# Performance work log

Measured on AMD Instinct MI355X. Metric: run time of the kernel, lower is better.

The kernel has to match this reference:

```python
import jax, jax.numpy as jnp
import numpy as np

NODE_DIM = 128
N_NODES = 100000
N_EDGES = 600000


def setup_inputs() -> dict:
    key = jax.random.key(0)
    k_x, k_e, k_w1, k_b1, k_w2, k_b2 = jax.random.split(key, 6)
    x = jax.random.normal(k_x, (N_NODES, NODE_DIM), dtype=jnp.float32)
    edge_index = jax.random.randint(k_e, (2, N_EDGES), 0, N_NODES, dtype=jnp.int64)
    # nn.Linear default init: U(-1/sqrt(fan_in), 1/sqrt(fan_in))
    lim1 = 1.0 / np.sqrt(2 * NODE_DIM)
    W1 = jax.random.uniform(k_w1, (2 * NODE_DIM, NODE_DIM), minval=-lim1, maxval=lim1, dtype=jnp.float32)
    b1 = jax.random.uniform(k_b1, (NODE_DIM,), minval=-lim1, maxval=lim1, dtype=jnp.float32)
    lim2 = 1.0 / np.sqrt(NODE_DIM)
    W2 = jax.random.uniform(k_w2, (NODE_DIM, 1), minval=-lim2, maxval=lim2, dtype=jnp.float32)
    b2 = jax.random.uniform(k_b2, (1,), minval=-lim2, maxval=lim2, dtype=jnp.float32)
    return {"x": x, "edge_index": edge_index, "W1": W1, "b1": b1, "W2": W2, "b2": b2}


def reference(x, edge_index, W1, b1, W2, b2):
    src = edge_index[0]
    dst = edge_index[1]
    # [E, 2*node_dim] gathered pair features
    pair = jnp.concatenate([x[src], x[dst]], axis=-1)
    h = jax.nn.relu(pair @ W1 + b1)          # [E, node_dim]
    s = jax.nn.sigmoid(h @ W2 + b2)          # [E, 1]
    return s.squeeze(-1)                      # [E]
```

## Files before the change

kernel.cpp:

```cpp
#include <hip/hip_runtime.h>
#include <hip/hip_bf16.h>
#include <stdint.h>

#define NODE_DIM 128
#define N_NODES  100000
#define N_EDGES  600000
#define NOUT     256

#define QSTEP_INV 64.0f
#define QSTEP     (1.0f / 64.0f)

typedef __bf16 bf16x8 __attribute__((ext_vector_type(8)));
typedef float  f32x4  __attribute__((ext_vector_type(4)));

static __device__ inline unsigned pack2_bf16(float a, float b) {
    unsigned short ua = __builtin_bit_cast(unsigned short, (__bf16)a);
    unsigned short ub = __builtin_bit_cast(unsigned short, (__bf16)b);
    return (unsigned)ua | ((unsigned)ub << 16);
}

static __device__ __forceinline__ void async_copy16(const float* g, void* l) {
    __builtin_amdgcn_global_load_lds(
        (__attribute__((address_space(1))) void*)(uintptr_t)g,
        (__attribute__((address_space(3))) void*)(uint32_t)(uintptr_t)l,
        16, 0, 0);
}

__global__ void wprep_kernel(const float* __restrict__ W1, __bf16* __restrict__ Wt) {
    int i = blockIdx.x * 256 + threadIdx.x;
    if (i >= NOUT * NODE_DIM) return;
    int kp = i >> 7;
    int n  = i & 127;
    float v = W1[i];
    int np = (kp < NODE_DIM) ? n  : (n + NODE_DIM);
    int k  = (kp < NODE_DIM) ? kp : (kp - NODE_DIM);
    Wt[np * NODE_DIM + k] = (__bf16)v;
}

#define MT   64
#define ELD  264

__global__ __launch_bounds__(256)
void gemm_pre_kernel(const float* __restrict__ x, const __bf16* __restrict__ Wt,
                     const float* __restrict__ b1,
                     unsigned char* __restrict__ Ai, unsigned char* __restrict__ Bi) {
    __shared__ __align__(16) char lds_raw[MT * ELD * 2];
    float* Xf = (float*)lds_raw;
    __bf16 (*Ls)[ELD] = (__bf16 (*)[ELD])lds_raw;

    const int t    = threadIdx.x;
    const int wave = t >> 6;
    const int lane = t & 63;
    const int lm   = lane & 15;
    const int q    = lane >> 4;
    const int m0   = blockIdx.x * MT;
    const int n0   = wave * 64;

#pragma unroll
    for (int i = 0; i < 8; ++i) {
        const int sbase = i * 256 + wave * 64;
        const int s  = sbase + lane;
        const int R  = s >> 5;
        const int p  = s & 31;
        const int cg = p ^ (R & 7);
        int gr = m0 + R;
        if (gr > N_NODES - 1) gr = N_NODES - 1;
        async_copy16(x + (size_t)gr * NODE_DIM + cg * 4, &Xf[(size_t)sbase * 4]);
    }

    bf16x8 bfr[4][4];
#pragma unroll
    for (int nt = 0; nt < 4; ++nt) {
        const int n = n0 + nt * 16 + lm;
#pragma unroll
        for (int ks = 0; ks < 4; ++ks)
            bfr[nt][ks] = __builtin_bit_cast(bf16x8,
                *(const uint4*)(Wt + (size_t)n * NODE_DIM + ks * 32 + q * 8));
    }

    __syncthreads();

    f32x4 acc[4][4];
#pragma unroll
    for (int i = 0; i < 4; ++i)
#pragma unroll
        for (int j = 0; j < 4; ++j)
            acc[i][j] = (f32x4){0.f, 0.f, 0.f, 0.f};

#pragma unroll
    for (int mt = 0; mt < 4; ++mt) {
        const int R  = mt * 16 + lm;
        const int rs = R & 7;
#pragma unroll
        for (int ks = 0; ks < 4; ++ks) {
            const int c0 = ks * 8 + q * 2;
            const float4 f0 = *(const float4*)&Xf[(R * 32 + (c0 ^ rs)) * 4];
            const float4 f1 = *(const float4*)&Xf[(R * 32 + ((c0 + 1) ^ rs)) * 4];
            uint4 p;
            p.x = pack2_bf16(f0.x, f0.y);
            p.y = pack2_bf16(f0.z, f0.w);
            p.z = pack2_bf16(f1.x, f1.y);
            p.w = pack2_bf16(f1.z, f1.w);
            bf16x8 af = __builtin_bit_cast(bf16x8, p);
#pragma unroll
            for (int nt = 0; nt < 4; ++nt)
                acc[mt][nt] = __builtin_amdgcn_mfma_f32_16x16x32_bf16(
                    af, bfr[nt][ks], acc[mt][nt], 0, 0, 0);
        }
    }

    __syncthreads();

#pragma unroll
    for (int nt = 0; nt < 4; ++nt) {
        const int n = n0 + nt * 16 + lm;
        const float bias = (n < NODE_DIM) ? b1[n] : 0.f;
#pragma unroll
        for (int mt = 0; mt < 4; ++mt) {
#pragma unroll
            for (int r = 0; r < 4; ++r)
                Ls[mt * 16 + q * 4 + r][n] = (__bf16)(acc[mt][nt][r] + bias);
        }
    }
    __syncthreads();

    const int grp = t >> 4;
    const int sub = t & 15;
#pragma unroll
    for (int pass = 0; pass < 8; ++pass) {
        const int hr   = pass * 16 + grp;
        const int row  = hr >> 1;
        const int half = hr & 1;
        const uint4 v = *(const uint4*)(&Ls[row][half * 128 + sub * 8]);
        const unsigned* vu = (const unsigned*)&v;
        unsigned u[8];
#pragma unroll
        for (int i = 0; i < 4; ++i) {
            const float fa = __builtin_bit_cast(float, vu[i] << 16);
            const float fb = __builtin_bit_cast(float, vu[i] & 0xffff0000u);
            float ga = fmaf(fa, QSTEP_INV, 128.5f);
            float gb = fmaf(fb, QSTEP_INV, 128.5f);
            ga = fminf(fmaxf(ga, 0.f), 255.f);
            gb = fminf(fmaxf(gb, 0.f), 255.f);
            u[2 * i]     = (unsigned)ga;
            u[2 * i + 1] = (unsigned)gb;
        }
        uint2 pk;
        pk.x = u[0] | (u[1] << 8) | (u[2] << 16) | (u[3] << 24);
        pk.y = u[4] | (u[5] << 8) | (u[6] << 16) | (u[7] << 24);
        const int m = m0 + row;
        if (m < N_NODES)
            *(uint2*)((half ? Bi : Ai) + (size_t)m * NODE_DIM + sub * 8) = pk;
    }
}

__global__ __launch_bounds__(256)
void edge_score_kernel(const unsigned char* __restrict__ Ai,
                       const unsigned char* __restrict__ Bi,
                       const int* __restrict__ idx,
                       const float* __restrict__ W2, const float* __restrict__ b2,
                       float* __restrict__ out) {
    const int t      = threadIdx.x;
    const int sub    = t & 15;
    const int g0     = (blockIdx.x * 256 + t) >> 4;
    const int stride = (gridDim.x * 256) >> 4;

    float w[8];
#pragma unroll
    for (int j = 0; j < 8; ++j) w[j] = W2[sub * 8 + j];
    const float bias2 = b2[0];

    for (int e = g0; e < N_EDGES; e += 2 * stride) {
        const int e1  = e + stride;
        const bool h1 = e1 < N_EDGES;
        const int s0 = idx[e];
        const int d0 = idx[N_EDGES + e];
        const int s1 = h1 ? idx[e1] : s0;
        const int d1 = h1 ? idx[N_EDGES + e1] : d0;

        const uint2 a0 = *(const uint2*)(Ai + (size_t)s0 * NODE_DIM + sub * 8);
        const uint2 b0 = *(const uint2*)(Bi + (size_t)d0 * NODE_DIM + sub * 8);
        const uint2 a1 = *(const uint2*)(Ai + (size_t)s1 * NODE_DIM + sub * 8);
        const uint2 b1v= *(const uint2*)(Bi + (size_t)d1 * NODE_DIM + sub * 8);

        const unsigned aw0[2] = {a0.x, a0.y}, bw0[2] = {b0.x, b0.y};
        const unsigned aw1[2] = {a1.x, a1.y}, bw1[2] = {b1v.x, b1v.y};
        float p0 = 0.f, p1 = 0.f;
#pragma unroll
        for (int wd = 0; wd < 2; ++wd) {
#pragma unroll
            for (int k = 0; k < 4; ++k) {
                const int ua0 = (int)((aw0[wd] >> (8 * k)) & 0xffu);
                const int ub0 = (int)((bw0[wd] >> (8 * k)) & 0xffu);
                const int ua1 = (int)((aw1[wd] >> (8 * k)) & 0xffu);
                const int ub1 = (int)((bw1[wd] >> (8 * k)) & 0xffu);
                const int r0 = max(ua0 + ub0, 256) - 256;
                const int r1 = max(ua1 + ub1, 256) - 256;
                p0 = fmaf((float)r0, w[wd * 4 + k], p0);
                p1 = fmaf((float)r1, w[wd * 4 + k], p1);
            }
        }
        p0 += __shfl_xor(p0, 1);  p1 += __shfl_xor(p1, 1);
        p0 += __shfl_xor(p0, 2);  p1 += __shfl_xor(p1, 2);
        p0 += __shfl_xor(p0, 4);  p1 += __shfl_xor(p1, 4);
        p0 += __shfl_xor(p0, 8);  p1 += __shfl_xor(p1, 8);
        if (sub == 0) {
            out[e] = 1.f / (1.f + __expf(-fmaf(p0, QSTEP, bias2)));
            if (h1) out[e1] = 1.f / (1.f + __expf(-fmaf(p1, QSTEP, bias2)));
        }
    }
}

__global__ __launch_bounds__(128)
void naive_edge_kernel(const float* __restrict__ x, const int* __restrict__ idx,
                       const float* __restrict__ W1, const float* __restrict__ b1,
                       const float* __restrict__ W2, const float* __restrict__ b2,
                       float* __restrict__ out) {
    __shared__ float pair[2 * NODE_DIM];
    __shared__ float red[2];
    int e = blockIdx.x;
    int t = threadIdx.x;
    int s = idx[e], d = idx[N_EDGES + e];
    pair[t]            = x[(size_t)s * NODE_DIM + t];
    pair[NODE_DIM + t] = x[(size_t)d * NODE_DIM + t];
    __syncthreads();
    float acc = b1[t];
    for (int k = 0; k < 2 * NODE_DIM; ++k)
        acc = fmaf(pair[k], W1[k * NODE_DIM + t], acc);
    float c = fmaxf(acc, 0.f) * W2[t];
#pragma unroll
    for (int m = 1; m < 64; m <<= 1) c += __shfl_xor(c, m);
    if ((t & 63) == 0) red[t >> 6] = c;
    __syncthreads();
    if (t == 0) out[e] = 1.f / (1.f + __expf(-(red[0] + red[1] + b2[0])));
}

extern "C" void kernel_launch(void* const* d_in, const int* in_sizes, int n_in,
                              void* d_out, int out_size, void* d_ws, size_t ws_size,
                              hipStream_t stream) {
    const float* x   = (const float*)d_in[0];
    const int*   idx = (const int*)d_in[1];
    const float* W1  = (const float*)d_in[2];
    const float* b1  = (const float*)d_in[3];
    const float* W2  = (const float*)d_in[4];
    const float* b2  = (const float*)d_in[5];
    float* out = (float*)d_out;

    const size_t tab_bytes = (size_t)N_NODES * NODE_DIM;
    const size_t wt_bytes  = (size_t)NOUT * NODE_DIM * sizeof(__bf16);
    const size_t need = 2 * tab_bytes + wt_bytes;

    if (ws_size >= need) {
        unsigned char* Ai = (unsigned char*)d_ws;
        unsigned char* Bi = Ai + tab_bytes;
        __bf16* Wt = (__bf16*)(Bi + tab_bytes);
        hipLaunchKernelGGL(wprep_kernel, dim3(128), dim3(256), 0, stream, W1, Wt);
        hipLaunchKernelGGL(gemm_pre_kernel, dim3((N_NODES + MT - 1) / MT), dim3(256),
                           0, stream, x, Wt, b1, Ai, Bi);
        hipLaunchKernelGGL(edge_score_kernel, dim3(2048), dim3(256), 0, stream,
                           Ai, Bi, idx, W2, b2, out);
    } else {
        hipLaunchKernelGGL(naive_edge_kernel, dim3(N_EDGES), dim3(128), 0, stream,
                           x, idx, W1, b1, W2, b2, out);
    }
}
```

Measured before the change: 138.5 us.

## Double-buffer two x tiles per GEMM block and widen edge-kernel gathers to 16 bytes

Each gemm_pre block now handles two 64-row tiles. The second tile's x load is issued into a separate 32KB LDS stage before the first tile is computed, so its DMA overlaps the first tile's MFMA and quantize work. This halves the grid size and spreads the B-fragment register loads over two tiles, but raises LDS use to 64KB per block, which may lower occupancy. Separately, the edge kernel uses 8 lanes per edge with 16-byte gathers instead of 16 lanes with 8-byte loads, which cuts the shuffle-reduction steps and gives fewer, wider memory transactions.

```diff
diff --git a/kernel.cpp b/kernel.cpp
--- a/kernel.cpp
+++ b/kernel.cpp
@@ -6,6 +6,7 @@
 #define N_NODES  100000
 #define N_EDGES  600000
 #define NOUT     256
+#define NTILES   1563
 
 #define QSTEP_INV 64.0f
 #define QSTEP     (1.0f / 64.0f)
@@ -24,6 +25,22 @@
         (__attribute__((address_space(1))) void*)(uintptr_t)g,
         (__attribute__((address_space(3))) void*)(uint32_t)(uintptr_t)l,
         16, 0, 0);
+}
+
+static __device__ __forceinline__ void dma_xtile(const float* __restrict__ x,
+                                                 char* stage, int m0,
+                                                 int wave, int lane) {
+#pragma unroll
+    for (int i = 0; i < 8; ++i) {
+        const int sbase = i * 256 + wave * 64;
+        const int s  = sbase + lane;
+        const int R  = s >> 5;
+        const int p  = s & 31;
+        const int cg = p ^ (R & 7);
+        int gr = m0 + R;
+        if (gr > N_NODES - 1) gr = N_NODES - 1;
+        async_copy16(x + (size_t)gr * NODE_DIM + cg * 4, stage + (size_t)s * 0 + (size_t)sbase * 16);
+    }
 }
 
 __global__ void wprep_kernel(const float* __restrict__ W1, __bf16* __restrict__ Wt) {
@@ -37,36 +54,24 @@
     Wt[np * NODE_DIM + k] = (__bf16)v;
 }
 
-#define MT   64
-#define ELD  264
+#define MT 64
 
 __global__ __launch_bounds__(256)
 void gemm_pre_kernel(const float* __restrict__ x, const __bf16* __restrict__ Wt,
                      const float* __restrict__ b1,
                      unsigned char* __restrict__ Ai, unsigned char* __restrict__ Bi) {
-    __shared__ __align__(16) char lds_raw[MT * ELD * 2];
-    float* Xf = (float*)lds_raw;
-    __bf16 (*Ls)[ELD] = (__bf16 (*)[ELD])lds_raw;
+    __shared__ __align__(16) char lds_raw[65536];
 
     const int t    = threadIdx.x;
     const int wave = t >> 6;
     const int lane = t & 63;
     const int lm   = lane & 15;
     const int q    = lane >> 4;
-    const int m0   = blockIdx.x * MT;
     const int n0   = wave * 64;
-
-#pragma unroll
-    for (int i = 0; i < 8; ++i) {
-        const int sbase = i * 256 + wave * 64;
-        const int s  = sbase + lane;
-        const int R  = s >> 5;
-        const int p  = s & 31;
-        const int cg = p ^ (R & 7);
-        int gr = m0 + R;
-        if (gr > N_NODES - 1) gr = N_NODES - 1;
-        async_copy16(x + (size_t)gr * NODE_DIM + cg * 4, &Xf[(size_t)sbase * 4]);
-    }
+    const int tile0 = blockIdx.x * 2;
+    const bool hasT1 = (tile0 + 1) < NTILES;
+
+    dma_xtile(x, lds_raw, tile0 * MT, wave, lane);
 
     bf16x8 bfr[4][4];
 #pragma unroll
@@ -80,77 +85,88 @@
 
     __syncthreads();
 
-    f32x4 acc[4][4];
-#pragma unroll
-    for (int i = 0; i < 4; ++i)
-#pragma unroll
-        for (int j = 0; j < 4; ++j)
-            acc[i][j] = (f32x4){0.f, 0.f, 0.f, 0.f};
-
-#pragma unroll
-    for (int mt = 0; mt < 4; ++mt) {
-        const int R  = mt * 16 + lm;
-        const int rs = R & 7;
-#pragma unroll
-        for (int ks = 0; ks < 4; ++ks) {
-            const int c0 = ks * 8 + q * 2;
-            const float4 f0 = *(const float4*)&Xf[(R * 32 + (c0 ^ rs)) * 4];
-            const float4 f1 = *(const float4*)&Xf[(R * 32 + ((c0 + 1) ^ rs)) * 4];
-            uint4 p;
-            p.x = pack2_bf16(f0.x, f0.y);
-            p.y = pack2_bf16(f0.z, f0.w);
-            p.z = pack2_bf16(f1.x, f1.y);
-            p.w = pack2_bf16(f1.z, f1.w);
-            bf16x8 af = __builtin_bit_cast(bf16x8, p);
-#pragma unroll
-            for (int nt = 0; nt < 4; ++nt)
-                acc[mt][nt] = __builtin_amdgcn_mfma_f32_16x16x32_bf16(
-                    af, bfr[nt][ks], acc[mt][nt], 0, 0, 0);
-        }
-    }
-
-    __syncthreads();
-
-#pragma unroll
-    for (int nt = 0; nt < 4; ++nt) {
-        const int n = n0 + nt * 16 + lm;
-        const float bias = (n < NODE_DIM) ? b1[n] : 0.f;
+    if (hasT1) dma_xtile(x, lds_raw + 32768, (tile0 + 1) * MT, wave, lane);
+
+#pragma unroll 1
+    for (int j = 0; j < 2; ++j) {
+        if (j == 1 && !hasT1) break;
+        char* stage = lds_raw + j * 32768;
+        const float* Xf = (const float*)stage;
+        __bf16 (*Ls)[256] = (__bf16 (*)[256])stage;
+        const int m0 = (tile0 + j) * MT;
+
+        f32x4 acc[4][4];
+#pragma unroll
+        for (int a = 0; a < 4; ++a)
+#pragma unroll
+            for (int b = 0; b < 4; ++b)
+                acc[a][b] = (f32x4){0.f, 0.f, 0.f, 0.f};
+
 #pragma unroll
         for (int mt = 0; mt < 4; ++mt) {
-#pragma unroll
-            for (int r = 0; r < 4; ++r)
-                Ls[mt * 16 + q * 4 + r][n] = (__bf16)(acc[mt][nt][r] + bias);
-        }
-    }
-    __syncthreads();
-
-    const int grp = t >> 4;
-    const int sub = t & 15;
-#pragma unroll
-    for (int pass = 0; pass < 8; ++pass) {
-        const int hr   = pass * 16 + grp;
-        const int row  = hr >> 1;
-        const int half = hr & 1;
-        const uint4 v = *(const uint4*)(&Ls[row][half * 128 + sub * 8]);
-        const unsigned* vu = (const unsigned*)&v;
-        unsigned u[8];
-#pragma unroll
-        for (int i = 0; i < 4; ++i) {
-            const float fa = __builtin_bit_cast(float, vu[i] << 16);
-            const float fb = __builtin_bit_cast(float, vu[i] & 0xffff0000u);
-            float ga = fmaf(fa, QSTEP_INV, 128.5f);
-            float gb = fmaf(fb, QSTEP_INV, 128.5f);
-            ga = fminf(fmaxf(ga, 0.f), 255.f);
-            gb = fminf(fmaxf(gb, 0.f), 255.f);
-            u[2 * i]     = (unsigned)ga;
-            u[2 * i + 1] = (unsigned)gb;
-        }
-        uint2 pk;
-        pk.x = u[0] | (u[1] << 8) | (u[2] << 16) | (u[3] << 24);
-        pk.y = u[4] | (u[5] << 8) | (u[6] << 16) | (u[7] << 24);
-        const int m = m0 + row;
-        if (m < N_NODES)
-            *(uint2*)((half ? Bi : Ai) + (size_t)m * NODE_DIM + sub * 8) = pk;
+            const int R  = mt * 16 + lm;
+            const int rs = R & 7;
+#pragma unroll
+            for (int ks = 0; ks < 4; ++ks) {
+                const int c0 = ks * 8 + q * 2;
+                const float4 f0 = *(const float4*)&Xf[(R * 32 + (c0 ^ rs)) * 4];
+                const float4 f1 = *(const float4*)&Xf[(R * 32 + ((c0 + 1) ^ rs)) * 4];
+                uint4 p;
+                p.x = pack2_bf16(f0.x, f0.y);
+                p.y = pack2_bf16(f0.z, f0.w);
+                p.z = pack2_bf16(f1.x, f1.y);
+                p.w = pack2_bf16(f1.z, f1.w);
+                bf16x8 af = __builtin_bit_cast(bf16x8, p);
+#pragma unroll
+                for (int nt = 0; nt < 4; ++nt)
+                    acc[mt][nt] = __builtin_amdgcn_mfma_f32_16x16x32_bf16(
+                        af, bfr[nt][ks], acc[mt][nt], 0, 0, 0);
+            }
+        }
+
+        __syncthreads();
+
+#pragma unroll
+        for (int nt = 0; nt < 4; ++nt) {
+            const int n = n0 + nt * 16 + lm;
+            const float bias = (n < NODE_DIM) ? b1[n] : 0.f;
+#pragma unroll
+            for (int mt = 0; mt < 4; ++mt) {
+#pragma unroll
+                for (int r = 0; r < 4; ++r)
+                    Ls[mt * 16 + q * 4 + r][n] = (__bf16)(acc[mt][nt][r] + bias);
+            }
+        }
+        __syncthreads();
+
+        const int grp = t >> 4;
+        const int sub = t & 15;
+#pragma unroll
+        for (int pass = 0; pass < 8; ++pass) {
+            const int hr   = pass * 16 + grp;
+            const int row  = hr >> 1;
+            const int half = hr & 1;
+            const uint4 v = *(const uint4*)(&Ls[row][half * 128 + sub * 8]);
+            const unsigned* vu = (const unsigned*)&v;
+            unsigned u[8];
+#pragma unroll
+            for (int i = 0; i < 4; ++i) {
+                const float fa = __builtin_bit_cast(float, vu[i] << 16);
+                const float fb = __builtin_bit_cast(float, vu[i] & 0xffff0000u);
+                float ga = fmaf(fa, QSTEP_INV, 128.5f);
+                float gb = fmaf(fb, QSTEP_INV, 128.5f);
+                ga = fminf(fmaxf(ga, 0.f), 255.f);
+                gb = fminf(fmaxf(gb, 0.f), 255.f);
+                u[2 * i]     = (unsigned)ga;
+                u[2 * i + 1] = (unsigned)gb;
+            }
+            uint2 pk;
+            pk.x = u[0] | (u[1] << 8) | (u[2] << 16) | (u[3] << 24);
+            pk.y = u[4] | (u[5] << 8) | (u[6] << 16) | (u[7] << 24);
+            const int m = m0 + row;
+            if (m < N_NODES)
+                *(uint2*)((half ? Bi : Ai) + (size_t)m * NODE_DIM + sub * 8) = pk;
+        }
     }
 }
 
@@ -161,13 +177,13 @@
                        const float* __restrict__ W2, const float* __restrict__ b2,
                        float* __restrict__ out) {
     const int t      = threadIdx.x;
-    const int sub    = t & 15;
-    const int g0     = (blockIdx.x * 256 + t) >> 4;
-    const int stride = (gridDim.x * 256) >> 4;
-
-    float w[8];
-#pragma unroll
-    for (int j = 0; j < 8; ++j) w[j] = W2[sub * 8 + j];
+    const int sub    = t & 7;
+    const int g0     = (blockIdx.x * 256 + t) >> 3;
+    const int stride = (gridDim.x * 256) >> 3;
+
+    float w[16];
+#pragma unroll
+    for (int j = 0; j < 16; ++j) w[j] = W2[sub * 16 + j];
     const float bias2 = b2[0];
 
     for (int e = g0; e < N_EDGES; e += 2 * stride) {
@@ -178,16 +194,18 @@
         const int s1 = h1 ? idx[e1] : s0;
         const int d1 = h1 ? idx[N_EDGES + e1] : d0;
 
-        const uint2 a0 = *(const uint2*)(Ai + (size_t)s0 * NODE_DIM + sub * 8);
-        const uint2 b0 = *(const uint2*)(Bi + (size_t)d0 * NODE_DIM + sub * 8);
-        const uint2 a1 = *(const uint2*)(Ai + (size_t)s1 * NODE_DIM + sub * 8);
-        const uint2 b1v= *(const uint2*)(Bi + (size_t)d1 * NODE_DIM + sub * 8);
-
-        const unsigned aw0[2] = {a0.x, a0.y}, bw0[2] = {b0.x, b0.y};
-        const unsigned aw1[2] = {a1.x, a1.y}, bw1[2] = {b1v.x, b1v.y};
+        const uint4 a0 = *(const uint4*)(Ai + (size_t)s0 * NODE_DIM + sub * 16);
+        const uint4 b0 = *(const uint4*)(Bi + (size_t)d0 * NODE_DIM + sub * 16);
+        const uint4 a1 = *(const uint4*)(Ai + (size_t)s1 * NODE_DIM + sub * 16);
+        const uint4 b1v= *(const uint4*)(Bi + (size_t)d1 * NODE_DIM + sub * 16);
+
+        const unsigned aw0[4] = {a0.x, a0.y, a0.z, a0.w};
+        const unsigned bw0[4] = {b0.x, b0.y, b0.z, b0.w};
+        const unsigned aw1[4] = {a1.x, a1.y, a1.z, a1.w};
+        const unsigned bw1[4] = {b1v.x, b1v.y, b1v.z, b1v.w};
         float p0 = 0.f, p1 = 0.f;
 #pragma unroll
-        for (int wd = 0; wd < 2; ++wd) {
+        for (int wd = 0; wd < 4; ++wd) {
 #pragma unroll
             for (int k = 0; k < 4; ++k) {
                 const int ua0 = (int)((aw0[wd] >> (8 * k)) & 0xffu);
@@ -203,7 +221,6 @@
         p0 += __shfl_xor(p0, 1);  p1 += __shfl_xor(p1, 1);
         p0 += __shfl_xor(p0, 2);  p1 += __shfl_xor(p1, 2);
         p0 += __shfl_xor(p0, 4);  p1 += __shfl_xor(p1, 4);
-        p0 += __shfl_xor(p0, 8);  p1 += __shfl_xor(p1, 8);
         if (sub == 0) {
             out[e] = 1.f / (1.f + __expf(-fmaf(p0, QSTEP, bias2)));
             if (h1) out[e1] = 1.f / (1.f + __expf(-fmaf(p1, QSTEP, bias2)));
@@ -255,7 +272,7 @@
         unsigned char* Bi = Ai + tab_bytes;
         __bf16* Wt = (__bf16*)(Bi + tab_bytes);
         hipLaunchKernelGGL(wprep_kernel, dim3(128), dim3(256), 0, stream, W1, Wt);
-        hipLaunchKernelGGL(gemm_pre_kernel, dim3((N_NODES + MT - 1) / MT), dim3(256),
+        hipLaunchKernelGGL(gemm_pre_kernel, dim3((NTILES + 1) / 2), dim3(256),
                            0, stream, x, Wt, b1, Ai, Bi);
         hipLaunchKernelGGL(edge_score_kernel, dim3(2048), dim3(256), 0, stream,
                            Ai, Bi, idx, W2, b2, out);
```

New measurement: 140.8 us. Within noise of the previous version (+1.6%).
